# Optimization experiments

Hardware: AMD Instinct MI355X
Metric: run time of the kernel (lower is better)

The kernel has to match this reference:

```python
import jax, jax.numpy as jnp
import numpy as np

N_NODES = 131072
N_EDGES = 2097152
IN_DIM = 768
HID = 64
NODES_PER_GRAPH = 32
OUT_DIM = 2


def setup_inputs() -> dict:
    key = jax.random.key(0)
    k1, k2, k3, k4 = jax.random.split(key, 4)
    x = jax.random.normal(k1, (N_NODES, IN_DIM), dtype=jnp.float32)
    edge_index = jax.random.randint(k2, (2, N_EDGES), 0, N_NODES, dtype=jnp.int64)
    W_conv = jax.random.normal(k3, (IN_DIM, HID), dtype=jnp.float32) * 0.02
    b_conv = jnp.zeros((HID,), dtype=jnp.float32)
    W_lin = jax.random.normal(k4, (OUT_DIM, HID * NODES_PER_GRAPH), dtype=jnp.float32) * 0.02
    b_lin = jnp.zeros((OUT_DIM,), dtype=jnp.float32)
    return {"x": x, "edge_index": edge_index, "W_conv": W_conv,
            "b_conv": b_conv, "W_lin": W_lin, "b_lin": b_lin}


def reference(x, edge_index, W_conv, b_conv, W_lin, b_lin):
    N = x.shape[0]
    # GCNConv: add self-loops, symmetric normalization D^-1/2 (A+I) D^-1/2
    loops = jnp.arange(N, dtype=edge_index.dtype)
    src = jnp.concatenate([edge_index[0], loops])  # [E+N]
    dst = jnp.concatenate([edge_index[1], loops])
    deg = jax.ops.segment_sum(jnp.ones_like(dst, dtype=x.dtype), dst, num_segments=N)
    dinv = jax.lax.rsqrt(deg)  # deg >= 1 due to self-loops
    norm = dinv[src] * dinv[dst]  # [E+N]
    h = x @ W_conv  # [N, HID]
    msg = h[src] * norm[:, None]  # gather + scale
    out = jax.ops.segment_sum(msg, dst, num_segments=N) + b_conv  # scatter-add
    out = jax.nn.relu(out)
    out = out.reshape(-1, HID * NODES_PER_GRAPH)  # [B, 2048]
    logits = out @ W_lin.T + b_lin  # [B, OUT_DIM]
    return jax.nn.log_softmax(logits, axis=1)
```

## Files before the change

kernel.cpp:

```cpp
#include <hip/hip_runtime.h>
#include <hip/hip_bf16.h>

#define N_NODES 131072
#define N_EDGES 2097152
#define IN_DIM 768
#define HID 64
#define NPG 32
#define NGRAPH (N_NODES / NPG)

#define BM 128
#define GEMM_BLOCKS (N_NODES / BM)

#define RNG 128
#define NB (N_NODES / RNG)
#define EPB 4096
#define NCB (N_EDGES / EPB)
#define PBLK 8
#define RPB (NCB / PBLK)
#define PREP_BLK 192

typedef __attribute__((ext_vector_type(8))) short bf16x8;
typedef __attribute__((ext_vector_type(4))) float f32x4;

static __device__ __forceinline__ unsigned short f2bf(float f) {
    __hip_bfloat16 h = __float2bfloat16(f);
    return *reinterpret_cast<unsigned short*>(&h);
}
static __device__ __forceinline__ float bf2f(unsigned short s) {
    return __uint_as_float(((unsigned int)s) << 16);
}

__global__ __launch_bounds__(256) void gcn_prep_count(const float* __restrict__ W,
                                                      unsigned short* __restrict__ Wt,
                                                      const int* __restrict__ dst,
                                                      unsigned int* __restrict__ C) {
    __shared__ unsigned int hist[NB];
    int tid = threadIdx.x;
    if (blockIdx.x < PREP_BLK) {
        int i = blockIdx.x * 256 + tid;
        if (i < IN_DIM * HID) {
            int k = i >> 6, n = i & 63;
            Wt[n * IN_DIM + k] = f2bf(W[i]);
        }
        return;
    }
    int cb = blockIdx.x - PREP_BLK;
    for (int t = tid; t < NB; t += 256) hist[t] = 0u;
    __syncthreads();
    int base = cb * EPB;
    #pragma unroll
    for (int u = 0; u < EPB / 256; ++u) {
        int d = dst[base + u * 256 + tid];
        atomicAdd(&hist[d >> 7], 1u);
    }
    __syncthreads();
    for (int t = tid; t < NB; t += 256) C[(size_t)cb * NB + t] = hist[t];
}

__global__ __launch_bounds__(256) void gcn_gemm_prefA(const float* __restrict__ x,
                                                      const unsigned short* __restrict__ Wt,
                                                      unsigned short* __restrict__ h,
                                                      unsigned int* __restrict__ C,
                                                      unsigned int* __restrict__ S) {
    int tid = threadIdx.x;

    if (blockIdx.x >= GEMM_BLOCKS) {
        int p = blockIdx.x - GEMM_BLOCKS;
        #pragma unroll
        for (int c = 0; c < 4; ++c) {
            int t = tid + c * 256;
            unsigned int run = 0;
            for (int r = 0; r < RPB; r += 8) {
                unsigned int v[8];
                size_t base = ((size_t)(p * RPB + r)) * NB + t;
                #pragma unroll
                for (int j = 0; j < 8; ++j) v[j] = C[base + (size_t)j * NB];
                #pragma unroll
                for (int j = 0; j < 8; ++j) { C[base + (size_t)j * NB] = run; run += v[j]; }
            }
            S[p * NB + t] = run;
        }
        return;
    }

    int lane = tid & 63;
    int w = tid >> 6;
    int rowbase = blockIdx.x * BM;
    int rl = lane & 15;
    int kq = (lane >> 4) * 8;

    const float* xa0 = x + (size_t)(rowbase + w * 32 + rl) * IN_DIM + kq;
    const float* xa1 = xa0 + (size_t)16 * IN_DIM;
    const unsigned short* wp = Wt + (size_t)rl * IN_DIM + kq;

    f32x4 acc[2][4] = {};

    #pragma unroll 2
    for (int kb = 0; kb < IN_DIM; kb += 32) {
        float4 u0 = *(const float4*)(xa0 + kb);
        float4 u1 = *(const float4*)(xa0 + kb + 4);
        float4 u2 = *(const float4*)(xa1 + kb);
        float4 u3 = *(const float4*)(xa1 + kb + 4);
        bf16x8 b0 = *(const bf16x8*)(wp + kb);
        bf16x8 b1 = *(const bf16x8*)(wp + (size_t)16 * IN_DIM + kb);
        bf16x8 b2 = *(const bf16x8*)(wp + (size_t)32 * IN_DIM + kb);
        bf16x8 b3 = *(const bf16x8*)(wp + (size_t)48 * IN_DIM + kb);
        bf16x8 a0, a1;
        a0[0] = (short)f2bf(u0.x); a0[1] = (short)f2bf(u0.y);
        a0[2] = (short)f2bf(u0.z); a0[3] = (short)f2bf(u0.w);
        a0[4] = (short)f2bf(u1.x); a0[5] = (short)f2bf(u1.y);
        a0[6] = (short)f2bf(u1.z); a0[7] = (short)f2bf(u1.w);
        a1[0] = (short)f2bf(u2.x); a1[1] = (short)f2bf(u2.y);
        a1[2] = (short)f2bf(u2.z); a1[3] = (short)f2bf(u2.w);
        a1[4] = (short)f2bf(u3.x); a1[5] = (short)f2bf(u3.y);
        a1[6] = (short)f2bf(u3.z); a1[7] = (short)f2bf(u3.w);
        acc[0][0] = __builtin_amdgcn_mfma_f32_16x16x32_bf16(a0, b0, acc[0][0], 0, 0, 0);
        acc[1][0] = __builtin_amdgcn_mfma_f32_16x16x32_bf16(a1, b0, acc[1][0], 0, 0, 0);
        acc[0][1] = __builtin_amdgcn_mfma_f32_16x16x32_bf16(a0, b1, acc[0][1], 0, 0, 0);
        acc[1][1] = __builtin_amdgcn_mfma_f32_16x16x32_bf16(a1, b1, acc[1][1], 0, 0, 0);
        acc[0][2] = __builtin_amdgcn_mfma_f32_16x16x32_bf16(a0, b2, acc[0][2], 0, 0, 0);
        acc[1][2] = __builtin_amdgcn_mfma_f32_16x16x32_bf16(a1, b2, acc[1][2], 0, 0, 0);
        acc[0][3] = __builtin_amdgcn_mfma_f32_16x16x32_bf16(a0, b3, acc[0][3], 0, 0, 0);
        acc[1][3] = __builtin_amdgcn_mfma_f32_16x16x32_bf16(a1, b3, acc[1][3], 0, 0, 0);
    }
    for (int rt = 0; rt < 2; ++rt) {
        int row0 = rowbase + w * 32 + rt * 16 + (lane >> 4) * 4;
        #pragma unroll
        for (int ct = 0; ct < 4; ++ct)
            #pragma unroll
            for (int rr = 0; rr < 4; ++rr) {
                int col = ct * 16 + (lane & 15);
                h[(size_t)(row0 + rr) * HID + col] = f2bf(acc[rt][ct][rr]);
            }
    }
}

__global__ __launch_bounds__(1024) void gcn_prefB(unsigned int* __restrict__ S,
                                                  unsigned int* __restrict__ bstart) {
    __shared__ unsigned int sc[NB];
    int t = threadIdx.x;
    unsigned int run = 0;
    unsigned int v[PBLK];
    #pragma unroll
    for (int p = 0; p < PBLK; ++p) v[p] = S[p * NB + t];
    #pragma unroll
    for (int p = 0; p < PBLK; ++p) { S[p * NB + t] = run; run += v[p]; }
    sc[t] = run;
    __syncthreads();
    for (int off = 1; off < NB; off <<= 1) {
        unsigned int u = (t >= off) ? sc[t - off] : 0u;
        __syncthreads();
        sc[t] += u;
        __syncthreads();
    }
    bstart[t] = sc[t] - run;
    if (t == NB - 1) bstart[NB] = sc[NB - 1];
}

__global__ __launch_bounds__(256) void gcn_scatter(const int* __restrict__ src,
                                                   const int* __restrict__ dst,
                                                   const unsigned int* __restrict__ C,
                                                   const unsigned int* __restrict__ S,
                                                   const unsigned int* __restrict__ bstart,
                                                   unsigned int* __restrict__ part) {
    __shared__ unsigned int off[NB];
    int tid = threadIdx.x, cb = blockIdx.x;
    int p = cb >> 6;
    for (int t = tid; t < NB; t += 256)
        off[t] = bstart[t] + S[p * NB + t] + C[(size_t)cb * NB + t];
    __syncthreads();
    int base = cb * EPB;
    #pragma unroll
    for (int u = 0; u < EPB / 256; ++u) {
        int i = base + u * 256 + tid;
        int d = dst[i];
        unsigned int pos = atomicAdd(&off[d >> 7], 1u);
        part[pos] = (unsigned int)src[i] | ((unsigned int)(d & (RNG - 1)) << 17);
    }
}

__global__ __launch_bounds__(256) void gcn_sort2(const unsigned int* __restrict__ part,
                                                 const unsigned int* __restrict__ bstart,
                                                 unsigned int* __restrict__ part2,
                                                 unsigned int* __restrict__ nstart,
                                                 float* __restrict__ dinv) {
    __shared__ unsigned int hist[RNG];
    __shared__ unsigned int sc[RNG];
    __shared__ unsigned int off[RNG];
    int tid = threadIdx.x, b = blockIdx.x;
    if (tid < RNG) hist[tid] = 0u;
    __syncthreads();
    unsigned int s0 = bstart[b], s1 = bstart[b + 1];
    for (unsigned int j = s0 + tid; j < s1; j += 256)
        atomicAdd(&hist[part[j] >> 17], 1u);
    __syncthreads();
    if (tid < RNG) sc[tid] = hist[tid];
    __syncthreads();
    #pragma unroll
    for (int o = 1; o < RNG; o <<= 1) {
        unsigned int u = (tid < RNG && tid >= o) ? sc[tid - o] : 0u;
        __syncthreads();
        if (tid < RNG) sc[tid] += u;
        __syncthreads();
    }
    if (tid < RNG) {
        unsigned int excl = sc[tid] - hist[tid];
        nstart[b * RNG + tid] = s0 + excl;
        off[tid] = s0 + excl;
        dinv[b * RNG + tid] = rsqrtf((float)(hist[tid] + 1));
    }
    if (b == NB - 1 && tid == 0) nstart[N_NODES] = N_EDGES;
    __syncthreads();
    for (unsigned int j = s0 + tid; j < s1; j += 256) {
        unsigned int pr = part[j];
        unsigned int pos = atomicAdd(&off[pr >> 17], 1u);
        part2[pos] = pr & 0x1FFFF;
    }
}

__global__ __launch_bounds__(512) void gcn_agg(const unsigned short* __restrict__ h,
                                               const unsigned int* __restrict__ part2,
                                               const unsigned int* __restrict__ nstart,
                                               const float* __restrict__ dinv,
                                               const float* __restrict__ b_conv,
                                               const float* __restrict__ W_lin,
                                               const float* __restrict__ b_lin,
                                               float* __restrict__ out) {
    __shared__ float p0s[8], p1s[8];
    int tid = threadIdx.x, lane = tid & 63, w = tid >> 6;
    int g = blockIdx.x;
    float bc = b_conv[lane];
    float l0 = 0.f, l1 = 0.f;

    #pragma unroll
    for (int k = 0; k < 4; ++k) {
        int node = w * 4 + k;
        int i = g * NPG + node;
        unsigned int st = nstart[i];
        unsigned int en = nstart[i + 1];
        int c = (int)(en - st);
        float di = dinv[i];
        float acc = di * bf2f(h[(size_t)i * HID + lane]);
        for (int base = 0; base < c; base += 64) {
            int m = min(64, c - base);
            int sidx = 0;
            float dsv = 0.f;
            if (lane < m) {
                sidx = (int)part2[st + base + lane];
                dsv = dinv[sidx];
            }
            int e = 0;
            for (; e + 4 <= m; e += 4) {
                int s0 = __shfl(sidx, e + 0);
                int s1 = __shfl(sidx, e + 1);
                int s2 = __shfl(sidx, e + 2);
                int s3 = __shfl(sidx, e + 3);
                float d0 = __shfl(dsv, e + 0);
                float d1 = __shfl(dsv, e + 1);
                float d2 = __shfl(dsv, e + 2);
                float d3 = __shfl(dsv, e + 3);
                float v0 = bf2f(h[(size_t)s0 * HID + lane]);
                float v1 = bf2f(h[(size_t)s1 * HID + lane]);
                float v2 = bf2f(h[(size_t)s2 * HID + lane]);
                float v3 = bf2f(h[(size_t)s3 * HID + lane]);
                acc = fmaf(d0, v0, acc);
                acc = fmaf(d1, v1, acc);
                acc = fmaf(d2, v2, acc);
                acc = fmaf(d3, v3, acc);
            }
            for (; e < m; ++e) {
                int s = __shfl(sidx, e);
                float ds = __shfl(dsv, e);
                acc = fmaf(ds, bf2f(h[(size_t)s * HID + lane]), acc);
            }
        }
        float v = fmaxf(fmaf(acc, di, bc), 0.f);
        l0 = fmaf(v, W_lin[node * HID + lane], l0);
        l1 = fmaf(v, W_lin[HID * NPG + node * HID + lane], l1);
    }
    #pragma unroll
    for (int d = 32; d > 0; d >>= 1) {
        l0 += __shfl_down(l0, d);
        l1 += __shfl_down(l1, d);
    }
    if (lane == 0) { p0s[w] = l0; p1s[w] = l1; }
    __syncthreads();
    if (tid == 0) {
        float A = b_lin[0], B = b_lin[1];
        #pragma unroll
        for (int j = 0; j < 8; ++j) { A += p0s[j]; B += p1s[j]; }
        float m = fmaxf(A, B);
        float lse = m + logf(expf(A - m) + expf(B - m));
        out[g * 2 + 0] = A - lse;
        out[g * 2 + 1] = B - lse;
    }
}

extern "C" void kernel_launch(void* const* d_in, const int* in_sizes, int n_in,
                              void* d_out, int out_size, void* d_ws, size_t ws_size,
                              hipStream_t stream) {
    const float* x  = (const float*)d_in[0];
    const int* ei   = (const int*)d_in[1];
    const float* Wc = (const float*)d_in[2];
    const float* bc = (const float*)d_in[3];
    const float* Wl = (const float*)d_in[4];
    const float* bl = (const float*)d_in[5];
    float* out = (float*)d_out;

    char* ws = (char*)d_ws;
    unsigned short* Wt   = (unsigned short*)(ws);
    float*          dinv = (float*)(ws + (128 << 10));
    unsigned int*  bstart= (unsigned int*)(ws + (640 << 10));
    unsigned int*  S     = (unsigned int*)(ws + (656 << 10));
    unsigned int*  C     = (unsigned int*)(ws + (1024 << 10));
    unsigned int*  part  = (unsigned int*)(ws + (3u << 20));
    unsigned short* h    = (unsigned short*)(ws + (11u << 20));
    unsigned int*  part2 = (unsigned int*)(ws + (27u << 20));
    unsigned int*  nstart= (unsigned int*)(ws + (35u << 20));

    const int* srcIdx = ei;
    const int* dstIdx = ei + N_EDGES;

    gcn_prep_count<<<PREP_BLK + NCB, 256, 0, stream>>>(Wc, Wt, dstIdx, C);
    gcn_gemm_prefA<<<GEMM_BLOCKS + PBLK, 256, 0, stream>>>(x, Wt, h, C, S);
    gcn_prefB<<<1, 1024, 0, stream>>>(S, bstart);
    gcn_scatter<<<NCB, 256, 0, stream>>>(srcIdx, dstIdx, C, S, bstart, part);
    gcn_sort2<<<NB, 256, 0, stream>>>(part, bstart, part2, nstart, dinv);
    gcn_agg<<<NGRAPH, 512, 0, stream>>>(h, part2, nstart, dinv, bc, Wl, bl, out);
}
```

Measured before the change: 259.6 us.

## Split GEMM into slices co-scheduled with each sort stage launch

The node-feature GEMM is split into four slices of 256 row blocks, and each slice is appended to one of the prefix-A, prefix-B, scatter and sort2 launches through a single multi-stage kernel. The latency-bound, low-occupancy sorting stages then overlap with compute-heavy GEMM work instead of running serially. The single-block prefB stage also drops from 1024 to 256 threads, with each thread handling four bins. In exchange the GEMM loses contiguity, and every stage kernel now carries the LDS footprint and register pressure of the shared kernel.

```diff
diff --git a/kernel.cpp b/kernel.cpp
--- a/kernel.cpp
+++ b/kernel.cpp
@@ -10,6 +10,7 @@
 
 #define BM 128
 #define GEMM_BLOCKS (N_NODES / BM)
+#define GSLICE 256
 
 #define RNG 128
 #define NB (N_NODES / RNG)
@@ -18,6 +19,11 @@
 #define PBLK 8
 #define RPB (NCB / PBLK)
 #define PREP_BLK 192
+
+#define ST_PREFA   0
+#define ST_PREFB   1
+#define ST_SCATTER 2
+#define ST_SORT2   3
 
 typedef __attribute__((ext_vector_type(8))) short bf16x8;
 typedef __attribute__((ext_vector_type(4))) float f32x4;
@@ -57,35 +63,124 @@
     for (int t = tid; t < NB; t += 256) C[(size_t)cb * NB + t] = hist[t];
 }
 
-__global__ __launch_bounds__(256) void gcn_gemm_prefA(const float* __restrict__ x,
-                                                      const unsigned short* __restrict__ Wt,
-                                                      unsigned short* __restrict__ h,
-                                                      unsigned int* __restrict__ C,
-                                                      unsigned int* __restrict__ S) {
+__global__ __launch_bounds__(256) void gcn_stage(int stage, int nStage, int gemmOfs,
+                                                 const float* __restrict__ x,
+                                                 const unsigned short* __restrict__ Wt,
+                                                 unsigned short* __restrict__ h,
+                                                 const int* __restrict__ src,
+                                                 const int* __restrict__ dst,
+                                                 unsigned int* __restrict__ C,
+                                                 unsigned int* __restrict__ S,
+                                                 unsigned int* __restrict__ bstart,
+                                                 unsigned int* __restrict__ part,
+                                                 unsigned int* __restrict__ part2,
+                                                 unsigned int* __restrict__ nstart,
+                                                 float* __restrict__ dinv) {
+    __shared__ unsigned int smem[NB];
     int tid = threadIdx.x;
 
-    if (blockIdx.x >= GEMM_BLOCKS) {
-        int p = blockIdx.x - GEMM_BLOCKS;
-        #pragma unroll
-        for (int c = 0; c < 4; ++c) {
-            int t = tid + c * 256;
-            unsigned int run = 0;
-            for (int r = 0; r < RPB; r += 8) {
-                unsigned int v[8];
-                size_t base = ((size_t)(p * RPB + r)) * NB + t;
+    if ((int)blockIdx.x < nStage) {
+        if (stage == ST_PREFA) {
+            int p = blockIdx.x;
+            #pragma unroll
+            for (int c = 0; c < 4; ++c) {
+                int t = tid + c * 256;
+                unsigned int run = 0;
+                for (int r = 0; r < RPB; r += 8) {
+                    unsigned int v[8];
+                    size_t base = ((size_t)(p * RPB + r)) * NB + t;
+                    #pragma unroll
+                    for (int j = 0; j < 8; ++j) v[j] = C[base + (size_t)j * NB];
+                    #pragma unroll
+                    for (int j = 0; j < 8; ++j) { C[base + (size_t)j * NB] = run; run += v[j]; }
+                }
+                S[p * NB + t] = run;
+            }
+        } else if (stage == ST_PREFB) {
+            unsigned int tot[4], lexcl[4];
+            unsigned int lrun = 0;
+            #pragma unroll
+            for (int j = 0; j < 4; ++j) {
+                unsigned int t = tid * 4 + j;
+                unsigned int r = 0;
                 #pragma unroll
-                for (int j = 0; j < 8; ++j) v[j] = C[base + (size_t)j * NB];
-                #pragma unroll
-                for (int j = 0; j < 8; ++j) { C[base + (size_t)j * NB] = run; run += v[j]; }
-            }
-            S[p * NB + t] = run;
+                for (int p = 0; p < PBLK; ++p) {
+                    unsigned int v = S[p * NB + t];
+                    S[p * NB + t] = r;
+                    r += v;
+                }
+                tot[j] = r;
+                lexcl[j] = lrun;
+                lrun += r;
+            }
+            smem[tid] = lrun;
+            __syncthreads();
+            for (int off = 1; off < 256; off <<= 1) {
+                unsigned int u = (tid >= off) ? smem[tid - off] : 0u;
+                __syncthreads();
+                smem[tid] += u;
+                __syncthreads();
+            }
+            unsigned int texcl = smem[tid] - lrun;
+            #pragma unroll
+            for (int j = 0; j < 4; ++j) bstart[tid * 4 + j] = texcl + lexcl[j];
+            if (tid == 255) bstart[NB] = N_EDGES;
+        } else if (stage == ST_SCATTER) {
+            unsigned int* off = smem;
+            int cb = blockIdx.x;
+            int p = cb >> 6;
+            for (int t = tid; t < NB; t += 256)
+                off[t] = bstart[t] + S[p * NB + t] + C[(size_t)cb * NB + t];
+            __syncthreads();
+            int base = cb * EPB;
+            #pragma unroll
+            for (int u = 0; u < EPB / 256; ++u) {
+                int i = base + u * 256 + tid;
+                int d = dst[i];
+                unsigned int pos = atomicAdd(&off[d >> 7], 1u);
+                part[pos] = (unsigned int)src[i] | ((unsigned int)(d & (RNG - 1)) << 17);
+            }
+        } else {
+            unsigned int* hist = smem;
+            unsigned int* sc   = smem + RNG;
+            unsigned int* off  = smem + 2 * RNG;
+            int b = blockIdx.x;
+            if (tid < RNG) hist[tid] = 0u;
+            __syncthreads();
+            unsigned int s0 = bstart[b], s1 = bstart[b + 1];
+            for (unsigned int j = s0 + tid; j < s1; j += 256)
+                atomicAdd(&hist[part[j] >> 17], 1u);
+            __syncthreads();
+            if (tid < RNG) sc[tid] = hist[tid];
+            __syncthreads();
+            #pragma unroll
+            for (int o = 1; o < RNG; o <<= 1) {
+                unsigned int u = (tid < RNG && tid >= o) ? sc[tid - o] : 0u;
+                __syncthreads();
+                if (tid < RNG) sc[tid] += u;
+                __syncthreads();
+            }
+            if (tid < RNG) {
+                unsigned int excl = sc[tid] - hist[tid];
+                nstart[b * RNG + tid] = s0 + excl;
+                off[tid] = s0 + excl;
+                dinv[b * RNG + tid] = rsqrtf((float)(hist[tid] + 1));
+            }
+            if (b == NB - 1 && tid == 0) nstart[N_NODES] = N_EDGES;
+            __syncthreads();
+            for (unsigned int j = s0 + tid; j < s1; j += 256) {
+                unsigned int pr = part[j];
+                unsigned int pos = atomicAdd(&off[pr >> 17], 1u);
+                part2[pos] = pr & 0x1FFFF;
+            }
         }
         return;
     }
 
+    int gb = gemmOfs + ((int)blockIdx.x - nStage);
     int lane = tid & 63;
     int w = tid >> 6;
-    int rowbase = blockIdx.x * BM;
+    int rowbase = gb * BM;
     int rl = lane & 15;
     int kq = (lane >> 4) * 8;
 
@@ -135,89 +230,6 @@
     }
 }
 
-__global__ __launch_bounds__(1024) void gcn_prefB(unsigned int* __restrict__ S,
-                                                  unsigned int* __restrict__ bstart) {
-    __shared__ unsigned int sc[NB];
-    int t = threadIdx.x;
-    unsigned int run = 0;
-    unsigned int v[PBLK];
-    #pragma unroll
-    for (int p = 0; p < PBLK; ++p) v[p] = S[p * NB + t];
-    #pragma unroll
-    for (int p = 0; p < PBLK; ++p) { S[p * NB + t] = run; run += v[p]; }
-    sc[t] = run;
-    __syncthreads();
-    for (int off = 1; off < NB; off <<= 1) {
-        unsigned int u = (t >= off) ? sc[t - off] : 0u;
-        __syncthreads();
-        sc[t] += u;
-        __syncthreads();
-    }
-    bstart[t] = sc[t] - run;
-    if (t == NB - 1) bstart[NB] = sc[NB - 1];
-}
-
-__global__ __launch_bounds__(256) void gcn_scatter(const int* __restrict__ src,
-                                                   const int* __restrict__ dst,
-                                                   const unsigned int* __restrict__ C,
-                                                   const unsigned int* __restrict__ S,
-                                                   const unsigned int* __restrict__ bstart,
-                                                   unsigned int* __restrict__ part) {
-    __shared__ unsigned int off[NB];
-    int tid = threadIdx.x, cb = blockIdx.x;
-    int p = cb >> 6;
-    for (int t = tid; t < NB; t += 256)
-        off[t] = bstart[t] + S[p * NB + t] + C[(size_t)cb * NB + t];
-    __syncthreads();
-    int base = cb * EPB;
-    #pragma unroll
-    for (int u = 0; u < EPB / 256; ++u) {
-        int i = base + u * 256 + tid;
-        int d = dst[i];
-        unsigned int pos = atomicAdd(&off[d >> 7], 1u);
-        part[pos] = (unsigned int)src[i] | ((unsigned int)(d & (RNG - 1)) << 17);
-    }
-}
-
-__global__ __launch_bounds__(256) void gcn_sort2(const unsigned int* __restrict__ part,
-                                                 const unsigned int* __restrict__ bstart,
-                                                 unsigned int* __restrict__ part2,
-                                                 unsigned int* __restrict__ nstart,
-                                                 float* __restrict__ dinv) {
-    __shared__ unsigned int hist[RNG];
-    __shared__ unsigned int sc[RNG];
-    __shared__ unsigned int off[RNG];
-    int tid = threadIdx.x, b = blockIdx.x;
-    if (tid < RNG) hist[tid] = 0u;
-    __syncthreads();
-    unsigned int s0 = bstart[b], s1 = bstart[b + 1];
-    for (unsigned int j = s0 + tid; j < s1; j += 256)
-        atomicAdd(&hist[part[j] >> 17], 1u);
-    __syncthreads();
-    if (tid < RNG) sc[tid] = hist[tid];
-    __syncthreads();
-    #pragma unroll
-    for (int o = 1; o < RNG; o <<= 1) {
-        unsigned int u = (tid < RNG && tid >= o) ? sc[tid - o] : 0u;
-        __syncthreads();
-        if (tid < RNG) sc[tid] += u;
-        __syncthreads();
-    }
-    if (tid < RNG) {
-        unsigned int excl = sc[tid] - hist[tid];
-        nstart[b * RNG + tid] = s0 + excl;
-        off[tid] = s0 + excl;
-        dinv[b * RNG + tid] = rsqrtf((float)(hist[tid] + 1));
-    }
-    if (b == NB - 1 && tid == 0) nstart[N_NODES] = N_EDGES;
-    __syncthreads();
-    for (unsigned int j = s0 + tid; j < s1; j += 256) {
-        unsigned int pr = part[j];
-        unsigned int pos = atomicAdd(&off[pr >> 17], 1u);
-        part2[pos] = pr & 0x1FFFF;
-    }
-}
-
 __global__ __launch_bounds__(512) void gcn_agg(const unsigned short* __restrict__ h,
                                                const unsigned int* __restrict__ part2,
                                                const unsigned int* __restrict__ nstart,
@@ -322,9 +334,13 @@
     const int* dstIdx = ei + N_EDGES;
 
     gcn_prep_count<<<PREP_BLK + NCB, 256, 0, stream>>>(Wc, Wt, dstIdx, C);
-    gcn_gemm_prefA<<<GEMM_BLOCKS + PBLK, 256, 0, stream>>>(x, Wt, h, C, S);
-    gcn_prefB<<<1, 1024, 0, stream>>>(S, bstart);
-    gcn_scatter<<<NCB, 256, 0, stream>>>(srcIdx, dstIdx, C, S, bstart, part);
-    gcn_sort2<<<NB, 256, 0, stream>>>(part, bstart, part2, nstart, dinv);
+    gcn_stage<<<PBLK + GSLICE, 256, 0, stream>>>(ST_PREFA, PBLK, 0 * GSLICE,
+        x, Wt, h, srcIdx, dstIdx, C, S, bstart, part, part2, nstart, dinv);
+    gcn_stage<<<1 + GSLICE, 256, 0, stream>>>(ST_PREFB, 1, 1 * GSLICE,
+        x, Wt, h, srcIdx, dstIdx, C, S, bstart, part, part2, nstart, dinv);
+    gcn_stage<<<NCB + GSLICE, 256, 0, stream>>>(ST_SCATTER, NCB, 2 * GSLICE,
+        x, Wt, h, srcIdx, dstIdx, C, S, bstart, part, part2, nstart, dinv);
+    gcn_stage<<<NB + GSLICE, 256, 0, stream>>>(ST_SORT2, NB, 3 * GSLICE,
+        x, Wt, h, srcIdx, dstIdx, C, S, bstart, part, part2, nstart, dinv);
     gcn_agg<<<NGRAPH, 512, 0, stream>>>(h, part2, nstart, dinv, bc, Wl, bl, out);
 }
```

Result: slower. 290.7 us (+12.0%).

## Move GEMM after sorting and pre-scale h by dinv in fp32

Applied to the files above, without the earlier changes.

The GEMM is split out of the prefix kernel and now runs after the CSR build, so each row of h can be multiplied by dinv and stored as fp32. Aggregation then becomes a plain sum with no per-edge dinv gather or shuffles, and it loads indices directly with an 8-wide unroll. The GEMM loop gains register double-buffered prefetch, and prefB is reworked to use 256 threads. In exchange, the GEMM no longer overlaps with the prefix scan, and the fp32 h doubles the bytes moved by the gather.

```diff
diff --git a/kernel.cpp b/kernel.cpp
--- a/kernel.cpp
+++ b/kernel.cpp
@@ -25,9 +25,6 @@
 static __device__ __forceinline__ unsigned short f2bf(float f) {
     __hip_bfloat16 h = __float2bfloat16(f);
     return *reinterpret_cast<unsigned short*>(&h);
-}
-static __device__ __forceinline__ float bf2f(unsigned short s) {
-    return __uint_as_float(((unsigned int)s) << 16);
 }
 
 __global__ __launch_bounds__(256) void gcn_prep_count(const float* __restrict__ W,
@@ -57,32 +54,125 @@
     for (int t = tid; t < NB; t += 256) C[(size_t)cb * NB + t] = hist[t];
 }
 
-__global__ __launch_bounds__(256) void gcn_gemm_prefA(const float* __restrict__ x,
-                                                      const unsigned short* __restrict__ Wt,
-                                                      unsigned short* __restrict__ h,
-                                                      unsigned int* __restrict__ C,
-                                                      unsigned int* __restrict__ S) {
+__global__ __launch_bounds__(256) void gcn_prefA(unsigned int* __restrict__ C,
+                                                 unsigned int* __restrict__ S) {
     int tid = threadIdx.x;
-
-    if (blockIdx.x >= GEMM_BLOCKS) {
-        int p = blockIdx.x - GEMM_BLOCKS;
+    int p = blockIdx.x;
+    #pragma unroll
+    for (int c = 0; c < 4; ++c) {
+        int t = tid + c * 256;
+        unsigned int run = 0;
+        for (int r = 0; r < RPB; r += 8) {
+            unsigned int v[8];
+            size_t base = ((size_t)(p * RPB + r)) * NB + t;
+            #pragma unroll
+            for (int j = 0; j < 8; ++j) v[j] = C[base + (size_t)j * NB];
+            #pragma unroll
+            for (int j = 0; j < 8; ++j) { C[base + (size_t)j * NB] = run; run += v[j]; }
+        }
+        S[p * NB + t] = run;
+    }
+}
+
+__global__ __launch_bounds__(256) void gcn_prefB(unsigned int* __restrict__ S,
+                                                 unsigned int* __restrict__ bstart) {
+    __shared__ unsigned int sm[256];
+    int tid = threadIdx.x;
+    unsigned int lexcl[4];
+    unsigned int lrun = 0;
+    #pragma unroll
+    for (int j = 0; j < 4; ++j) {
+        unsigned int t = tid * 4 + j;
+        unsigned int r = 0;
         #pragma unroll
-        for (int c = 0; c < 4; ++c) {
-            int t = tid + c * 256;
-            unsigned int run = 0;
-            for (int r = 0; r < RPB; r += 8) {
-                unsigned int v[8];
-                size_t base = ((size_t)(p * RPB + r)) * NB + t;
-                #pragma unroll
-                for (int j = 0; j < 8; ++j) v[j] = C[base + (size_t)j * NB];
-                #pragma unroll
-                for (int j = 0; j < 8; ++j) { C[base + (size_t)j * NB] = run; run += v[j]; }
-            }
-            S[p * NB + t] = run;
-        }
-        return;
-    }
-
+        for (int p = 0; p < PBLK; ++p) {
+            unsigned int v = S[p * NB + t];
+            S[p * NB + t] = r;
+            r += v;
+        }
+        lexcl[j] = lrun;
+        lrun += r;
+    }
+    sm[tid] = lrun;
+    __syncthreads();
+    for (int off = 1; off < 256; off <<= 1) {
+        unsigned int u = (tid >= off) ? sm[tid - off] : 0u;
+        __syncthreads();
+        sm[tid] += u;
+        __syncthreads();
+    }
+    unsigned int texcl = sm[tid] - lrun;
+    #pragma unroll
+    for (int j = 0; j < 4; ++j) bstart[tid * 4 + j] = texcl + lexcl[j];
+    if (tid == 255) bstart[NB] = N_EDGES;
+}
+
+__global__ __launch_bounds__(256) void gcn_scatter(const int* __restrict__ src,
+                                                   const int* __restrict__ dst,
+                                                   const unsigned int* __restrict__ C,
+                                                   const unsigned int* __restrict__ S,
+                                                   const unsigned int* __restrict__ bstart,
+                                                   unsigned int* __restrict__ part) {
+    __shared__ unsigned int off[NB];
+    int tid = threadIdx.x, cb = blockIdx.x;
+    int p = cb >> 6;
+    for (int t = tid; t < NB; t += 256)
+        off[t] = bstart[t] + S[p * NB + t] + C[(size_t)cb * NB + t];
+    __syncthreads();
+    int base = cb * EPB;
+    #pragma unroll
+    for (int u = 0; u < EPB / 256; ++u) {
+        int i = base + u * 256 + tid;
+        int d = dst[i];
+        unsigned int pos = atomicAdd(&off[d >> 7], 1u);
+        part[pos] = (unsigned int)src[i] | ((unsigned int)(d & (RNG - 1)) << 17);
+    }
+}
+
+__global__ __launch_bounds__(256) void gcn_sort2(const unsigned int* __restrict__ part,
+                                                 const unsigned int* __restrict__ bstart,
+                                                 unsigned int* __restrict__ part2,
+                                                 unsigned int* __restrict__ nstart,
+                                                 float* __restrict__ dinv) {
+    __shared__ unsigned int hist[RNG];
+    __shared__ unsigned int sc[RNG];
+    __shared__ unsigned int off[RNG];
+    int tid = threadIdx.x, b = blockIdx.x;
+    if (tid < RNG) hist[tid] = 0u;
+    __syncthreads();
+    unsigned int s0 = bstart[b], s1 = bstart[b + 1];
+    for (unsigned int j = s0 + tid; j < s1; j += 256)
+        atomicAdd(&hist[part[j] >> 17], 1u);
+    __syncthreads();
+    if (tid < RNG) sc[tid] = hist[tid];
+    __syncthreads();
+    #pragma unroll
+    for (int o = 1; o < RNG; o <<= 1) {
+        unsigned int u = (tid < RNG && tid >= o) ? sc[tid - o] : 0u;
+        __syncthreads();
+        if (tid < RNG) sc[tid] += u;
+        __syncthreads();
+    }
+    if (tid < RNG) {
+        unsigned int excl = sc[tid] - hist[tid];
+        nstart[b * RNG + tid] = s0 + excl;
+        off[tid] = s0 + excl;
+        dinv[b * RNG + tid] = rsqrtf((float)(hist[tid] + 1));
+    }
+    if (b == NB - 1 && tid == 0) nstart[N_NODES] = N_EDGES;
+    __syncthreads();
+    for (unsigned int j = s0 + tid; j < s1; j += 256) {
+        unsigned int pr = part[j];
+        unsigned int pos = atomicAdd(&off[pr >> 17], 1u);
+        part2[pos] = pr & 0x1FFFF;
+    }
+}
+
+__global__ __launch_bounds__(256) void gcn_gemm(const float* __restrict__ x,
+                                                const unsigned short* __restrict__ Wt,
+                                                const float* __restrict__ dinv,
+                                                float* __restrict__ hs) {
+    int tid = threadIdx.x;
     int lane = tid & 63;
     int w = tid >> 6;
     int rowbase = blockIdx.x * BM;
@@ -95,16 +185,32 @@
 
     f32x4 acc[2][4] = {};
 
-    #pragma unroll 2
+    float4 u0 = *(const float4*)(xa0);
+    float4 u1 = *(const float4*)(xa0 + 4);
+    float4 u2 = *(const float4*)(xa1);
+    float4 u3 = *(const float4*)(xa1 + 4);
+    bf16x8 b0 = *(const bf16x8*)(wp);
+    bf16x8 b1 = *(const bf16x8*)(wp + (size_t)16 * IN_DIM);
+    bf16x8 b2 = *(const bf16x8*)(wp + (size_t)32 * IN_DIM);
+    bf16x8 b3 = *(const bf16x8*)(wp + (size_t)48 * IN_DIM);
+
+    #pragma unroll 1
     for (int kb = 0; kb < IN_DIM; kb += 32) {
-        float4 u0 = *(const float4*)(xa0 + kb);
-        float4 u1 = *(const float4*)(xa0 + kb + 4);
-        float4 u2 = *(const float4*)(xa1 + kb);
-        float4 u3 = *(const float4*)(xa1 + kb + 4);
-        bf16x8 b0 = *(const bf16x8*)(wp + kb);
-        bf16x8 b1 = *(const bf16x8*)(wp + (size_t)16 * IN_DIM + kb);
-        bf16x8 b2 = *(const bf16x8*)(wp + (size_t)32 * IN_DIM + kb);
-        bf16x8 b3 = *(const bf16x8*)(wp + (size_t)48 * IN_DIM + kb);
+        float4 n0, n1, n2, n3;
+        bf16x8 c0, c1, c2, c3;
+        if (kb + 32 < IN_DIM) {
+            n0 = *(const float4*)(xa0 + kb + 32);
+            n1 = *(const float4*)(xa0 + kb + 36);
+            n2 = *(const float4*)(xa1 + kb + 32);
+            n3 = *(const float4*)(xa1 + kb + 36);
+            c0 = *(const bf16x8*)(wp + kb + 32);
+            c1 = *(const bf16x8*)(wp + (size_t)16 * IN_DIM + kb + 32);
+            c2 = *(const bf16x8*)(wp + (size_t)32 * IN_DIM + kb + 32);
+            c3 = *(const bf16x8*)(wp + (size_t)48 * IN_DIM + kb + 32);
+        } else {
+            n0 = u0; n1 = u1; n2 = u2; n3 = u3;
+            c0 = b0; c1 = b1; c2 = b2; c3 = b3;
+        }
         bf16x8 a0, a1;
         a0[0] = (short)f2bf(u0.x); a0[1] = (short)f2bf(u0.y);
         a0[2] = (short)f2bf(u0.z); a0[3] = (short)f2bf(u0.w);
@@ -122,103 +228,26 @@
         acc[1][2] = __builtin_amdgcn_mfma_f32_16x16x32_bf16(a1, b2, acc[1][2], 0, 0, 0);
         acc[0][3] = __builtin_amdgcn_mfma_f32_16x16x32_bf16(a0, b3, acc[0][3], 0, 0, 0);
         acc[1][3] = __builtin_amdgcn_mfma_f32_16x16x32_bf16(a1, b3, acc[1][3], 0, 0, 0);
-    }
+        u0 = n0; u1 = n1; u2 = n2; u3 = n3;
+        b0 = c0; b1 = c1; b2 = c2; b3 = c3;
+    }
+
+    #pragma unroll
     for (int rt = 0; rt < 2; ++rt) {
         int row0 = rowbase + w * 32 + rt * 16 + (lane >> 4) * 4;
         #pragma unroll
-        for (int ct = 0; ct < 4; ++ct)
+        for (int rr = 0; rr < 4; ++rr) {
+            float dv = dinv[row0 + rr];
             #pragma unroll
-            for (int rr = 0; rr < 4; ++rr) {
-                int col = ct * 16 + (lane & 15);
-                h[(size_t)(row0 + rr) * HID + col] = f2bf(acc[rt][ct][rr]);
+            for (int ct = 0; ct < 4; ++ct) {
+                int col = ct * 16 + rl;
+                hs[(size_t)(row0 + rr) * HID + col] = acc[rt][ct][rr] * dv;
             }
-    }
-}
-
-__global__ __launch_bounds__(1024) void gcn_prefB(unsigned int* __restrict__ S,
-                                                  unsigned int* __restrict__ bstart) {
-    __shared__ unsigned int sc[NB];
-    int t = threadIdx.x;
-    unsigned int run = 0;
-    unsigned int v[PBLK];
-    #pragma unroll
-    for (int p = 0; p < PBLK; ++p) v[p] = S[p * NB + t];
-    #pragma unroll
-    for (int p = 0; p < PBLK; ++p) { S[p * NB + t] = run; run += v[p]; }
-    sc[t] = run;
-    __syncthreads();
-    for (int off = 1; off < NB; off <<= 1) {
-        unsigned int u = (t >= off) ? sc[t - off] : 0u;
-        __syncthreads();
-        sc[t] += u;
-        __syncthreads();
-    }
-    bstart[t] = sc[t] - run;
-    if (t == NB - 1) bstart[NB] = sc[NB - 1];
-}
-
-__global__ __launch_bounds__(256) void gcn_scatter(const int* __restrict__ src,
-                                                   const int* __restrict__ dst,
-                                                   const unsigned int* __restrict__ C,
-                                                   const unsigned int* __restrict__ S,
-                                                   const unsigned int* __restrict__ bstart,
-                                                   unsigned int* __restrict__ part) {
-    __shared__ unsigned int off[NB];
-    int tid = threadIdx.x, cb = blockIdx.x;
-    int p = cb >> 6;
-    for (int t = tid; t < NB; t += 256)
-        off[t] = bstart[t] + S[p * NB + t] + C[(size_t)cb * NB + t];
-    __syncthreads();
-    int base = cb * EPB;
-    #pragma unroll
-    for (int u = 0; u < EPB / 256; ++u) {
-        int i = base + u * 256 + tid;
-        int d = dst[i];
-        unsigned int pos = atomicAdd(&off[d >> 7], 1u);
-        part[pos] = (unsigned int)src[i] | ((unsigned int)(d & (RNG - 1)) << 17);
-    }
-}
-
-__global__ __launch_bounds__(256) void gcn_sort2(const unsigned int* __restrict__ part,
-                                                 const unsigned int* __restrict__ bstart,
-                                                 unsigned int* __restrict__ part2,
-                                                 unsigned int* __restrict__ nstart,
-                                                 float* __restrict__ dinv) {
-    __shared__ unsigned int hist[RNG];
-    __shared__ unsigned int sc[RNG];
-    __shared__ unsigned int off[RNG];
-    int tid = threadIdx.x, b = blockIdx.x;
-    if (tid < RNG) hist[tid] = 0u;
-    __syncthreads();
-    unsigned int s0 = bstart[b], s1 = bstart[b + 1];
-    for (unsigned int j = s0 + tid; j < s1; j += 256)
-        atomicAdd(&hist[part[j] >> 17], 1u);
-    __syncthreads();
-    if (tid < RNG) sc[tid] = hist[tid];
-    __syncthreads();
-    #pragma unroll
-    for (int o = 1; o < RNG; o <<= 1) {
-        unsigned int u = (tid < RNG && tid >= o) ? sc[tid - o] : 0u;
-        __syncthreads();
-        if (tid < RNG) sc[tid] += u;
-        __syncthreads();
-    }
-    if (tid < RNG) {
-        unsigned int excl = sc[tid] - hist[tid];
-        nstart[b * RNG + tid] = s0 + excl;
-        off[tid] = s0 + excl;
-        dinv[b * RNG + tid] = rsqrtf((float)(hist[tid] + 1));
-    }
-    if (b == NB - 1 && tid == 0) nstart[N_NODES] = N_EDGES;
-    __syncthreads();
-    for (unsigned int j = s0 + tid; j < s1; j += 256) {
-        unsigned int pr = part[j];
-        unsigned int pos = atomicAdd(&off[pr >> 17], 1u);
-        part2[pos] = pr & 0x1FFFF;
-    }
-}
-
-__global__ __launch_bounds__(512) void gcn_agg(const unsigned short* __restrict__ h,
+        }
+    }
+}
+
+__global__ __launch_bounds__(512) void gcn_agg(const float* __restrict__ hs,
                                                const unsigned int* __restrict__ part2,
                                                const unsigned int* __restrict__ nstart,
                                                const float* __restrict__ dinv,
@@ -240,39 +269,42 @@
         unsigned int en = nstart[i + 1];
         int c = (int)(en - st);
         float di = dinv[i];
-        float acc = di * bf2f(h[(size_t)i * HID + lane]);
-        for (int base = 0; base < c; base += 64) {
-            int m = min(64, c - base);
-            int sidx = 0;
-            float dsv = 0.f;
-            if (lane < m) {
-                sidx = (int)part2[st + base + lane];
-                dsv = dinv[sidx];
-            }
-            int e = 0;
-            for (; e + 4 <= m; e += 4) {
-                int s0 = __shfl(sidx, e + 0);
-                int s1 = __shfl(sidx, e + 1);
-                int s2 = __shfl(sidx, e + 2);
-                int s3 = __shfl(sidx, e + 3);
-                float d0 = __shfl(dsv, e + 0);
-                float d1 = __shfl(dsv, e + 1);
-                float d2 = __shfl(dsv, e + 2);
-                float d3 = __shfl(dsv, e + 3);
-                float v0 = bf2f(h[(size_t)s0 * HID + lane]);
-                float v1 = bf2f(h[(size_t)s1 * HID + lane]);
-                float v2 = bf2f(h[(size_t)s2 * HID + lane]);
-                float v3 = bf2f(h[(size_t)s3 * HID + lane]);
-                acc = fmaf(d0, v0, acc);
-                acc = fmaf(d1, v1, acc);
-                acc = fmaf(d2, v2, acc);
-                acc = fmaf(d3, v3, acc);
-            }
-            for (; e < m; ++e) {
-                int s = __shfl(sidx, e);
-                float ds = __shfl(dsv, e);
-                acc = fmaf(ds, bf2f(h[(size_t)s * HID + lane]), acc);
-            }
+        float acc = hs[(size_t)i * HID + lane];
+        int e = 0;
+        for (; e + 8 <= c; e += 8) {
+            unsigned int s0 = part2[st + e + 0];
+            unsigned int s1 = part2[st + e + 1];
+            unsigned int s2 = part2[st + e + 2];
+            unsigned int s3 = part2[st + e + 3];
+            unsigned int s4 = part2[st + e + 4];
+            unsigned int s5 = part2[st + e + 5];
+            unsigned int s6 = part2[st + e + 6];
+            unsigned int s7 = part2[st + e + 7];
+            float v0 = hs[(size_t)s0 * HID + lane];
+            float v1 = hs[(size_t)s1 * HID + lane];
+            float v2 = hs[(size_t)s2 * HID + lane];
+            float v3 = hs[(size_t)s3 * HID + lane];
+            float v4 = hs[(size_t)s4 * HID + lane];
+            float v5 = hs[(size_t)s5 * HID + lane];
+            float v6 = hs[(size_t)s6 * HID + lane];
+            float v7 = hs[(size_t)s7 * HID + lane];
+            acc += v0; acc += v1; acc += v2; acc += v3;
+            acc += v4; acc += v5; acc += v6; acc += v7;
+        }
+        for (; e + 4 <= c; e += 4) {
+            unsigned int s0 = part2[st + e + 0];
+            unsigned int s1 = part2[st + e + 1];
+            unsigned int s2 = part2[st + e + 2];
+            unsigned int s3 = part2[st + e + 3];
+            float v0 = hs[(size_t)s0 * HID + lane];
+            float v1 = hs[(size_t)s1 * HID + lane];
+            float v2 = hs[(size_t)s2 * HID + lane];
+            float v3 = hs[(size_t)s3 * HID + lane];
+            acc += v0; acc += v1; acc += v2; acc += v3;
+        }
+        for (; e < c; ++e) {
+            unsigned int s = part2[st + e];
+            acc += hs[(size_t)s * HID + lane];
         }
         float v = fmaxf(fmaf(acc, di, bc), 0.f);
         l0 = fmaf(v, W_lin[node * HID + lane], l0);
@@ -312,19 +344,20 @@
     float*          dinv = (float*)(ws + (128 << 10));
     unsigned int*  bstart= (unsigned int*)(ws + (640 << 10));
     unsigned int*  S     = (unsigned int*)(ws + (656 << 10));
-    unsigned int*  C     = (unsigned int*)(ws + (1024 << 10));
-    unsigned int*  part  = (unsigned int*)(ws + (3u << 20));
-    unsigned short* h    = (unsigned short*)(ws + (11u << 20));
-    unsigned int*  part2 = (unsigned int*)(ws + (27u << 20));
-    unsigned int*  nstart= (unsigned int*)(ws + (35u << 20));
+    unsigned int*  part2 = (unsigned int*)(ws + (1u << 20));
+    unsigned int*  nstart= (unsigned int*)(ws + (9u << 20));
+    unsigned int*  C     = (unsigned int*)(ws + (10u << 20));
+    unsigned int*  part  = (unsigned int*)(ws + (12u << 20));
+    float*         hs    = (float*)(ws + (10u << 20));
 
     const int* srcIdx = ei;
     const int* dstIdx = ei + N_EDGES;
 
     gcn_prep_count<<<PREP_BLK + NCB, 256, 0, stream>>>(Wc, Wt, dstIdx, C);
-    gcn_gemm_prefA<<<GEMM_BLOCKS + PBLK, 256, 0, stream>>>(x, Wt, h, C, S);
-    gcn_prefB<<<1, 1024, 0, stream>>>(S, bstart);
+    gcn_prefA<<<PBLK, 256, 0, stream>>>(C, S);
+    gcn_prefB<<<1, 256, 0, stream>>>(S, bstart);
     gcn_scatter<<<NCB, 256, 0, stream>>>(srcIdx, dstIdx, C, S, bstart, part);
     gcn_sort2<<<NB, 256, 0, stream>>>(part, bstart, part2, nstart, dinv);
-    gcn_agg<<<NGRAPH, 512, 0, stream>>>(h, part2, nstart, dinv, bc, Wl, bl, out);
-}
+    gcn_gemm<<<GEMM_BLOCKS, 256, 0, stream>>>(x, Wt, dinv, hs);
+    gcn_agg<<<NGRAPH, 512, 0, stream>>>(hs, part2, nstart, dinv, bc, Wl, bl, out);
+}
```

After: 282.6 us. +8.9%, slower.
